# Performance work log

Hardware: AMD Instinct MI355X
Metric: run time of the kernel (lower is better)

The kernel has to match this reference:

```python
import jax, jax.numpy as jnp
import numpy as np

N = 50000
E = 800000
D_IN = 256
D_OUT = 256
ALPHA = 0.5


def setup_inputs() -> dict:
    key = jax.random.key(0)
    k1, k2, k3, k4, k5, k6 = jax.random.split(key, 6)
    stdv = 1.0 / np.sqrt(D_OUT)
    return {
        "input": jax.random.normal(k1, (N, D_IN), dtype=jnp.float32),
        "adj_src": jax.random.randint(k2, (E,), 0, N, dtype=jnp.int64),
        "adj_dst": jax.random.randint(k3, (E,), 0, N, dtype=jnp.int64),
        "adj_w": jax.random.uniform(k4, (E,), dtype=jnp.float32),
        "init_input": jax.random.normal(k5, (N, D_OUT), dtype=jnp.float32),
        "weight": jax.random.uniform(k6, (D_IN, D_OUT), dtype=jnp.float32,
                                     minval=-stdv, maxval=stdv),
    }


def reference(input, adj_src, adj_dst, adj_w, init_input, weight):
    # support = input @ W          [N, D_OUT] (dense GEMM)
    support = jnp.matmul(input, weight)
    # spmm: out[dst] += w * support[src]   (COO aggregate)
    msgs = support[adj_src] * adj_w[:, None]          # [E, D_OUT]
    agg = jax.ops.segment_sum(msgs, adj_dst, num_segments=N)  # [N, D_OUT]
    # alpha-blended residual + ReLU (bias=False, act=ReLU)
    out = agg * ALPHA + init_input * (1.0 - ALPHA)
    return jax.nn.relu(out)
```

## Files before the change

kernel.cpp:

```cpp
#include <hip/hip_runtime.h>
#include <hip/hip_fp16.h>

#define ALPHA 0.5f

typedef short short8v __attribute__((ext_vector_type(8)));
typedef float f32x4 __attribute__((ext_vector_type(4)));

__device__ __forceinline__ unsigned short f2bf(float f) {
  union { float f; unsigned u; } v; v.f = f;
  unsigned r = v.u + 0x7FFFu + ((v.u >> 16) & 1u);
  return (unsigned short)(r >> 16);
}
__device__ __forceinline__ float bf2f(unsigned short u) {
  union { unsigned u; float f; } v; v.u = ((unsigned)u) << 16;
  return v.f;
}
__device__ __forceinline__ float unpack_w(unsigned p) {
  return __half2float(__ushort_as_half((unsigned short)((p & 0x7FFFu) << 1)));
}

__global__ __launch_bounds__(256) void prep_small(
    const float* __restrict__ W, unsigned short* __restrict__ Wt,
    int* __restrict__ deg, int N) {
  const int tid = threadIdx.x;
  const int bid = blockIdx.x;
  if (bid < 256) {
    __shared__ float tile[16][17];
    const int kb = (bid & 15) * 16, nb = (bid >> 4) * 16;
    const int tx = tid & 15, ty = tid >> 4;
    tile[ty][tx] = W[(kb + ty) * 256 + nb + tx];
    __syncthreads();
    Wt[(nb + ty) * 256 + kb + tx] = f2bf(tile[tx][ty]);
  } else {
    const int i4 = (bid - 256) * 256 + tid;
    const int base = i4 * 4;
    if (base + 3 < N) *reinterpret_cast<int4*>(&deg[base]) = make_int4(0, 0, 0, 0);
    else for (int j = 0; j < 4; ++j) if (base + j < N) deg[base + j] = 0;
  }
}

__global__ __launch_bounds__(256) void gemm_hist(
    const float* __restrict__ A, const unsigned short* __restrict__ Wt,
    unsigned short* __restrict__ C, int M,
    const int* __restrict__ dst, int* __restrict__ deg, int E, int GB, int HB) {
  __shared__ char smem[2][24576];
  const int tid = threadIdx.x;
  const int bid = blockIdx.x;

  if (bid >= GB) {
    const int hgid = (bid - GB) * 256 + tid;
    const int hstride = HB * 256;
    const int E4 = E & ~3;
    for (int i = hgid * 4; i < E4; i += hstride * 4) {
      int4 d = *reinterpret_cast<const int4*>(&dst[i]);
      atomicAdd(&deg[d.x], 1); atomicAdd(&deg[d.y], 1);
      atomicAdd(&deg[d.z], 1); atomicAdd(&deg[d.w], 1);
    }
    if (hgid < (E - E4)) atomicAdd(&deg[dst[E4 + hgid]], 1);
    return;
  }

  const int lane = tid & 63;
  const int w = tid >> 6;
  const int wm = w >> 1, wn = w & 1;
  const int row0 = bid * 128;

  f32x4 acc[4][8];
  #pragma unroll
  for (int m = 0; m < 4; ++m)
    #pragma unroll
    for (int n = 0; n < 8; ++n) acc[m][n] = (f32x4){0.f, 0.f, 0.f, 0.f};

  const int aR = tid >> 1;
  const int aKs = (tid & 1) * 16;
  const int aRow = (row0 + aR < M) ? (row0 + aR) : (M - 1);
  const float* aP = A + (size_t)aRow * 256 + aKs;
  const int aWrOff = (aR >> 4) * 1024 + (aKs >> 3) * 256 + (aR & 15) * 16;

  int cur = 0;
  {
    float4 av[4];
    #pragma unroll
    for (int j = 0; j < 4; ++j) av[j] = *reinterpret_cast<const float4*>(aP + j * 4);
    #pragma unroll
    for (int i = 0; i < 4; ++i) {
      int s = w * 4 + i;
      const unsigned short* g = Wt + (size_t)(s * 16 + (lane & 15)) * 256 + (lane >> 4) * 8;
      __builtin_amdgcn_global_load_lds(
          (const __attribute__((address_space(1))) void*)g,
          (__attribute__((address_space(3))) void*)(&smem[0][8192 + s * 1024]),
          16, 0, 0);
    }
    unsigned short ab[16];
    #pragma unroll
    for (int j = 0; j < 4; ++j) {
      ab[j * 4 + 0] = f2bf(av[j].x); ab[j * 4 + 1] = f2bf(av[j].y);
      ab[j * 4 + 2] = f2bf(av[j].z); ab[j * 4 + 3] = f2bf(av[j].w);
    }
    *reinterpret_cast<short8v*>(&smem[0][aWrOff])       = *reinterpret_cast<short8v*>(&ab[0]);
    *reinterpret_cast<short8v*>(&smem[0][aWrOff + 256]) = *reinterpret_cast<short8v*>(&ab[8]);
    __syncthreads();
  }

  #pragma unroll
  for (int t = 0; t < 8; ++t) {
    float4 av[4];
    const bool pf = (t < 7);
    if (pf) {
      const int k0 = (t + 1) * 32;
      #pragma unroll
      for (int j = 0; j < 4; ++j) av[j] = *reinterpret_cast<const float4*>(aP + k0 + j * 4);
      #pragma unroll
      for (int i = 0; i < 4; ++i) {
        int s = w * 4 + i;
        const unsigned short* g = Wt + (size_t)(s * 16 + (lane & 15)) * 256 + k0 + (lane >> 4) * 8;
        __builtin_amdgcn_global_load_lds(
            (const __attribute__((address_space(1))) void*)g,
            (__attribute__((address_space(3))) void*)(&smem[cur ^ 1][8192 + s * 1024]),
            16, 0, 0);
      }
    }
    short8v af[4], bfv[8];
    #pragma unroll
    for (int m = 0; m < 4; ++m)
      af[m] = *reinterpret_cast<const short8v*>(&smem[cur][(wm * 4 + m) * 1024 + lane * 16]);
    #pragma unroll
    for (int n = 0; n < 8; ++n)
      bfv[n] = *reinterpret_cast<const short8v*>(&smem[cur][8192 + (wn * 8 + n) * 1024 + lane * 16]);
    #pragma unroll
    for (int m = 0; m < 4; ++m)
      #pragma unroll
      for (int n = 0; n < 8; ++n)
        acc[m][n] = __builtin_amdgcn_mfma_f32_16x16x32_bf16(af[m], bfv[n], acc[m][n], 0, 0, 0);
    if (pf) {
      unsigned short ab[16];
      #pragma unroll
      for (int j = 0; j < 4; ++j) {
        ab[j * 4 + 0] = f2bf(av[j].x); ab[j * 4 + 1] = f2bf(av[j].y);
        ab[j * 4 + 2] = f2bf(av[j].z); ab[j * 4 + 3] = f2bf(av[j].w);
      }
      *reinterpret_cast<short8v*>(&smem[cur ^ 1][aWrOff])       = *reinterpret_cast<short8v*>(&ab[0]);
      *reinterpret_cast<short8v*>(&smem[cur ^ 1][aWrOff + 256]) = *reinterpret_cast<short8v*>(&ab[8]);
    }
    __syncthreads();
    cur ^= 1;
  }

  #pragma unroll
  for (int m = 0; m < 4; ++m) {
    #pragma unroll
    for (int n = 0; n < 8; ++n) {
      const int col = wn * 128 + n * 16 + (lane & 15);
      #pragma unroll
      for (int r = 0; r < 4; ++r) {
        const int row = row0 + wm * 64 + m * 16 + (lane >> 4) * 4 + r;
        if (row < M) C[(size_t)row * 256 + col] = f2bf(acc[m][n][r]);
      }
    }
  }
}

__global__ __launch_bounds__(256) void scan_pass1(const int* __restrict__ deg,
                                                  int* __restrict__ excl,
                                                  int* __restrict__ partial, int N) {
  const int tid = threadIdx.x;
  const int base = blockIdx.x * 1024 + tid * 4;
  int4 v = make_int4(0, 0, 0, 0);
  if (base + 3 < N) v = *reinterpret_cast<const int4*>(&deg[base]);
  else {
    if (base + 0 < N) v.x = deg[base + 0];
    if (base + 1 < N) v.y = deg[base + 1];
    if (base + 2 < N) v.z = deg[base + 2];
  }
  const int s = v.x + v.y + v.z + v.w;
  const int lane = tid & 63, wid = tid >> 6;
  int ps = s;
  #pragma unroll
  for (int off = 1; off < 64; off <<= 1) {
    int t = __shfl_up(ps, off, 64);
    if (lane >= off) ps += t;
  }
  __shared__ int wsum[4];
  if (lane == 63) wsum[wid] = ps;
  __syncthreads();
  int woff = 0;
  #pragma unroll
  for (int w2 = 0; w2 < 4; ++w2) woff += (w2 < wid) ? wsum[w2] : 0;
  const int texcl = woff + ps - s;
  int4 e = make_int4(texcl, texcl + v.x, texcl + v.x + v.y, texcl + v.x + v.y + v.z);
  if (base + 3 < N) *reinterpret_cast<int4*>(&excl[base]) = e;
  else {
    if (base + 0 < N) excl[base + 0] = e.x;
    if (base + 1 < N) excl[base + 1] = e.y;
    if (base + 2 < N) excl[base + 2] = e.z;
  }
  if (tid == 255) partial[blockIdx.x] = woff + ps;
}

__global__ __launch_bounds__(256) void scan_pass2(const int* __restrict__ excl,
                                                  const int* __restrict__ partial,
                                                  int* __restrict__ row_ptr,
                                                  int* __restrict__ cursor,
                                                  int N, int NB, int E) {
  __shared__ int s_off;
  const int tid = threadIdx.x;
  if (tid < 64) {
    int v = (tid < NB && tid < (int)blockIdx.x) ? partial[tid] : 0;
    #pragma unroll
    for (int off = 1; off < 64; off <<= 1) v += __shfl_xor(v, off, 64);
    if (tid == 0) s_off = v;
  }
  if (blockIdx.x == 0 && tid == 0) row_ptr[N] = E;
  __syncthreads();
  const int off = s_off;
  const int base = blockIdx.x * 1024 + tid * 4;
  if (base + 3 < N) {
    int4 v = *reinterpret_cast<const int4*>(&excl[base]);
    v.x += off; v.y += off; v.z += off; v.w += off;
    *reinterpret_cast<int4*>(&row_ptr[base]) = v;
    *reinterpret_cast<int4*>(&cursor[base]) = v;
  } else {
    for (int j = 0; j < 4; ++j)
      if (base + j < N) { int v = excl[base + j] + off; row_ptr[base + j] = v; cursor[base + j] = v; }
  }
}

__global__ __launch_bounds__(256) void reindex_edges(
    const int* __restrict__ src, const int* __restrict__ dst,
    const float* __restrict__ w, int* __restrict__ cursor,
    unsigned* __restrict__ edges, int E) {
  int i = (blockIdx.x * blockDim.x + threadIdx.x) * 4;
  if (i + 3 < E) {
    int4 sv = *reinterpret_cast<const int4*>(&src[i]);
    int4 dv = *reinterpret_cast<const int4*>(&dst[i]);
    float4 wv = *reinterpret_cast<const float4*>(&w[i]);
    int s_[4] = {sv.x, sv.y, sv.z, sv.w};
    int d_[4] = {dv.x, dv.y, dv.z, dv.w};
    float w_[4] = {wv.x, wv.y, wv.z, wv.w};
    #pragma unroll
    for (int j = 0; j < 4; ++j) {
      int slot = atomicAdd(&cursor[d_[j]], 1);
      unsigned hb = __half_as_ushort(__float2half(w_[j] * ALPHA));
      edges[slot] = ((unsigned)s_[j] << 15) | (hb >> 1);
    }
  } else {
    for (; i < E; ++i) {
      int slot = atomicAdd(&cursor[dst[i]], 1);
      unsigned hb = __half_as_ushort(__float2half(w[i] * ALPHA));
      edges[slot] = ((unsigned)src[i] << 15) | (hb >> 1);
    }
  }
}

__global__ __launch_bounds__(256) void aggregate(
    const unsigned short* __restrict__ support,
    const int* __restrict__ row_ptr,
    const unsigned* __restrict__ edges,
    const float* __restrict__ init, float* __restrict__ out, int N) {
  int node = blockIdx.x * 4 + (threadIdx.x >> 6);
  if (node >= N) return;
  int lane = threadIdx.x & 63;
  int start = row_ptr[node];
  int cnt = row_ptr[node + 1] - start;

  float4 ini = *reinterpret_cast<const float4*>(&init[(size_t)node * 256 + lane * 4]);

  float4 acc = make_float4(0.f, 0.f, 0.f, 0.f);
  int e = 0;
  for (; e + 7 < cnt; e += 8) {
    unsigned p[8];
    #pragma unroll
    for (int j = 0; j < 8; ++j) p[j] = edges[start + e + j];
    ushort4 v[8];
    #pragma unroll
    for (int j = 0; j < 8; ++j)
      v[j] = *reinterpret_cast<const ushort4*>(&support[(size_t)(p[j] >> 15) * 256 + lane * 4]);
    #pragma unroll
    for (int j = 0; j < 8; ++j) {
      float wj = unpack_w(p[j]);
      acc.x += wj * bf2f(v[j].x);
      acc.y += wj * bf2f(v[j].y);
      acc.z += wj * bf2f(v[j].z);
      acc.w += wj * bf2f(v[j].w);
    }
  }
  for (; e < cnt; ++e) {
    unsigned p = edges[start + e];
    ushort4 v = *reinterpret_cast<const ushort4*>(&support[(size_t)(p >> 15) * 256 + lane * 4]);
    float wj = unpack_w(p);
    acc.x += wj * bf2f(v.x); acc.y += wj * bf2f(v.y);
    acc.z += wj * bf2f(v.z); acc.w += wj * bf2f(v.w);
  }
  float4 o;
  o.x = fmaxf(acc.x + (1.f - ALPHA) * ini.x, 0.f);
  o.y = fmaxf(acc.y + (1.f - ALPHA) * ini.y, 0.f);
  o.z = fmaxf(acc.z + (1.f - ALPHA) * ini.z, 0.f);
  o.w = fmaxf(acc.w + (1.f - ALPHA) * ini.w, 0.f);
  *reinterpret_cast<float4*>(&out[(size_t)node * 256 + lane * 4]) = o;
}

extern "C" void kernel_launch(void* const* d_in, const int* in_sizes, int n_in,
                              void* d_out, int out_size, void* d_ws, size_t ws_size,
                              hipStream_t stream) {
  const float* input   = (const float*)d_in[0];
  const int*   adj_src = (const int*)d_in[1];
  const int*   adj_dst = (const int*)d_in[2];
  const float* adj_w   = (const float*)d_in[3];
  const float* init_in = (const float*)d_in[4];
  const float* weight  = (const float*)d_in[5];
  float* out = (float*)d_out;

  const int N = in_sizes[0] / 256;
  const int E = in_sizes[1];

  char* ws = (char*)d_ws;
  unsigned short* support = (unsigned short*)ws; ws += (size_t)N * 256 * 2;
  unsigned short* Wt      = (unsigned short*)ws; ws += 256 * 256 * 2;
  int* deg     = (int*)ws; ws += (size_t)N * 4;
  int* row_ptr = (int*)ws; ws += (size_t)(N + 1) * 4;
  int* cursor  = (int*)ws; ws += (size_t)N * 4;
  int* excl    = (int*)ws; ws += (size_t)N * 4;
  int* partial = (int*)ws; ws += 256;
  unsigned* edges = (unsigned*)ws; ws += (size_t)E * 4;

  const int NB = (N + 1023) / 1024;
  const int GB = (N + 127) / 128;
  const int HB = 800;

  prep_small<<<256 + (N / 4 + 255) / 256, 256, 0, stream>>>(weight, Wt, deg, N);

  gemm_hist<<<GB + HB, 256, 0, stream>>>(input, Wt, support, N,
                                         adj_dst, deg, E, GB, HB);

  scan_pass1<<<NB, 256, 0, stream>>>(deg, excl, partial, N);
  scan_pass2<<<NB, 256, 0, stream>>>(excl, partial, row_ptr, cursor, N, NB, E);
  reindex_edges<<<(E / 4 + 255) / 256, 256, 0, stream>>>(adj_src, adj_dst, adj_w, cursor, edges, E);

  aggregate<<<(N + 3) / 4, 256, 0, stream>>>(support, row_ptr, edges, init_in, out, N);
}
```

Measured before the change: 173.2 us.

## Merge scan passes into lookback scan and precompute bf16 residual alongside GEMM

Replaces the two-kernel prefix scan over node degrees with a single-pass decoupled lookback scan using global flags, removing one launch and the intermediate buffer. Adds extra blocks to the GEMM/histogram launch that convert init_input to pre-scaled bf16, so the aggregate kernel reads half the residual bytes. The conversion adds extra global traffic that must overlap with the GEMM to pay off, and the residual loses precision by being stored in bf16. The histogram block count is reduced to make room.

```diff
diff --git a/kernel.cpp b/kernel.cpp
--- a/kernel.cpp
+++ b/kernel.cpp
@@ -21,7 +21,7 @@
 
 __global__ __launch_bounds__(256) void prep_small(
     const float* __restrict__ W, unsigned short* __restrict__ Wt,
-    int* __restrict__ deg, int N) {
+    int* __restrict__ deg, int* __restrict__ scanmeta, int N) {
   const int tid = threadIdx.x;
   const int bid = blockIdx.x;
   if (bid < 256) {
@@ -32,8 +32,8 @@
     __syncthreads();
     Wt[(nb + ty) * 256 + kb + tx] = f2bf(tile[tx][ty]);
   } else {
-    const int i4 = (bid - 256) * 256 + tid;
-    const int base = i4 * 4;
+    if (bid == 256 && tid < 128) scanmeta[tid] = 0;
+    const int base = ((bid - 256) * 256 + tid) * 4;
     if (base + 3 < N) *reinterpret_cast<int4*>(&deg[base]) = make_int4(0, 0, 0, 0);
     else for (int j = 0; j < 4; ++j) if (base + j < N) deg[base + j] = 0;
   }
@@ -42,11 +42,28 @@
 __global__ __launch_bounds__(256) void gemm_hist(
     const float* __restrict__ A, const unsigned short* __restrict__ Wt,
     unsigned short* __restrict__ C, int M,
-    const int* __restrict__ dst, int* __restrict__ deg, int E, int GB, int HB) {
+    const int* __restrict__ dst, int* __restrict__ deg, int E,
+    const float* __restrict__ init, unsigned short* __restrict__ init_bf, int n8i,
+    int GB, int HB, int CB) {
   __shared__ char smem[2][24576];
   const int tid = threadIdx.x;
   const int bid = blockIdx.x;
 
+  if (bid >= GB + HB) {
+    const int cgid = (bid - GB - HB) * 256 + tid;
+    const int cstride = CB * 256;
+    for (int i = cgid; i < n8i; i += cstride) {
+      float4 a = *reinterpret_cast<const float4*>(&init[i * 8]);
+      float4 b = *reinterpret_cast<const float4*>(&init[i * 8 + 4]);
+      unsigned short o[8] = {
+        f2bf(a.x * (1.f - ALPHA)), f2bf(a.y * (1.f - ALPHA)),
+        f2bf(a.z * (1.f - ALPHA)), f2bf(a.w * (1.f - ALPHA)),
+        f2bf(b.x * (1.f - ALPHA)), f2bf(b.y * (1.f - ALPHA)),
+        f2bf(b.z * (1.f - ALPHA)), f2bf(b.w * (1.f - ALPHA))};
+      *reinterpret_cast<short8v*>(&init_bf[i * 8]) = *reinterpret_cast<short8v*>(o);
+    }
+    return;
+  }
   if (bid >= GB) {
     const int hgid = (bid - GB) * 256 + tid;
     const int hstride = HB * 256;
@@ -160,11 +177,16 @@
   }
 }
 
-__global__ __launch_bounds__(256) void scan_pass1(const int* __restrict__ deg,
-                                                  int* __restrict__ excl,
-                                                  int* __restrict__ partial, int N) {
+__global__ __launch_bounds__(256) void scan_lookback(
+    const int* __restrict__ deg, int* __restrict__ row_ptr, int* __restrict__ cursor,
+    int* __restrict__ scanmeta ,
+    int N, int E, int NB) {
+  int* flags = scanmeta;
+  int* aggv  = scanmeta + 64;
   const int tid = threadIdx.x;
-  const int base = blockIdx.x * 1024 + tid * 4;
+  const int bid = blockIdx.x;
+  const int base = bid * 1024 + tid * 4;
+
   int4 v = make_int4(0, 0, 0, 0);
   if (base + 3 < N) v = *reinterpret_cast<const int4*>(&deg[base]);
   else {
@@ -181,47 +203,44 @@
     if (lane >= off) ps += t;
   }
   __shared__ int wsum[4];
+  __shared__ int s_off;
   if (lane == 63) wsum[wid] = ps;
   __syncthreads();
   int woff = 0;
   #pragma unroll
   for (int w2 = 0; w2 < 4; ++w2) woff += (w2 < wid) ? wsum[w2] : 0;
   const int texcl = woff + ps - s;
-  int4 e = make_int4(texcl, texcl + v.x, texcl + v.x + v.y, texcl + v.x + v.y + v.z);
-  if (base + 3 < N) *reinterpret_cast<int4*>(&excl[base]) = e;
-  else {
-    if (base + 0 < N) excl[base + 0] = e.x;
-    if (base + 1 < N) excl[base + 1] = e.y;
-    if (base + 2 < N) excl[base + 2] = e.z;
-  }
-  if (tid == 255) partial[blockIdx.x] = woff + ps;
-}
-
-__global__ __launch_bounds__(256) void scan_pass2(const int* __restrict__ excl,
-                                                  const int* __restrict__ partial,
-                                                  int* __restrict__ row_ptr,
-                                                  int* __restrict__ cursor,
-                                                  int N, int NB, int E) {
-  __shared__ int s_off;
-  const int tid = threadIdx.x;
+
+  if (tid == 0) {
+    int total = wsum[0] + wsum[1] + wsum[2] + wsum[3];
+    atomicExch(&aggv[bid], total);
+    __threadfence();
+    atomicExch(&flags[bid], 1);
+  }
+  if (bid == 0 && tid == 0) row_ptr[N] = E;
+
   if (tid < 64) {
-    int v = (tid < NB && tid < (int)blockIdx.x) ? partial[tid] : 0;
-    #pragma unroll
-    for (int off = 1; off < 64; off <<= 1) v += __shfl_xor(v, off, 64);
-    if (tid == 0) s_off = v;
-  }
-  if (blockIdx.x == 0 && tid == 0) row_ptr[N] = E;
+    int a = 0;
+    if (tid < bid) {
+      while (atomicAdd(&flags[tid], 0) == 0) { }
+      a = atomicAdd(&aggv[tid], 0);
+    }
+    #pragma unroll
+    for (int m = 1; m < 64; m <<= 1) a += __shfl_xor(a, m, 64);
+    if (tid == 0) s_off = a;
+  }
   __syncthreads();
   const int off = s_off;
-  const int base = blockIdx.x * 1024 + tid * 4;
+
+  int4 e = make_int4(texcl + off, texcl + off + v.x,
+                     texcl + off + v.x + v.y, texcl + off + v.x + v.y + v.z);
   if (base + 3 < N) {
-    int4 v = *reinterpret_cast<const int4*>(&excl[base]);
-    v.x += off; v.y += off; v.z += off; v.w += off;
-    *reinterpret_cast<int4*>(&row_ptr[base]) = v;
-    *reinterpret_cast<int4*>(&cursor[base]) = v;
+    *reinterpret_cast<int4*>(&row_ptr[base]) = e;
+    *reinterpret_cast<int4*>(&cursor[base]) = e;
   } else {
+    int ev[4] = {e.x, e.y, e.z, e.w};
     for (int j = 0; j < 4; ++j)
-      if (base + j < N) { int v = excl[base + j] + off; row_ptr[base + j] = v; cursor[base + j] = v; }
+      if (base + j < N) { row_ptr[base + j] = ev[j]; cursor[base + j] = ev[j]; }
   }
 }
 
@@ -256,14 +275,14 @@
     const unsigned short* __restrict__ support,
     const int* __restrict__ row_ptr,
     const unsigned* __restrict__ edges,
-    const float* __restrict__ init, float* __restrict__ out, int N) {
+    const unsigned short* __restrict__ init_bf, float* __restrict__ out, int N) {
   int node = blockIdx.x * 4 + (threadIdx.x >> 6);
   if (node >= N) return;
   int lane = threadIdx.x & 63;
   int start = row_ptr[node];
   int cnt = row_ptr[node + 1] - start;
 
-  float4 ini = *reinterpret_cast<const float4*>(&init[(size_t)node * 256 + lane * 4]);
+  ushort4 ib = *reinterpret_cast<const ushort4*>(&init_bf[(size_t)node * 256 + lane * 4]);
 
   float4 acc = make_float4(0.f, 0.f, 0.f, 0.f);
   int e = 0;
@@ -292,10 +311,10 @@
     acc.z += wj * bf2f(v.z); acc.w += wj * bf2f(v.w);
   }
   float4 o;
-  o.x = fmaxf(acc.x + (1.f - ALPHA) * ini.x, 0.f);
-  o.y = fmaxf(acc.y + (1.f - ALPHA) * ini.y, 0.f);
-  o.z = fmaxf(acc.z + (1.f - ALPHA) * ini.z, 0.f);
-  o.w = fmaxf(acc.w + (1.f - ALPHA) * ini.w, 0.f);
+  o.x = fmaxf(acc.x + bf2f(ib.x), 0.f);
+  o.y = fmaxf(acc.y + bf2f(ib.y), 0.f);
+  o.z = fmaxf(acc.z + bf2f(ib.z), 0.f);
+  o.w = fmaxf(acc.w + bf2f(ib.w), 0.f);
   *reinterpret_cast<float4*>(&out[(size_t)node * 256 + lane * 4]) = o;
 }
 
@@ -315,26 +334,29 @@
 
   char* ws = (char*)d_ws;
   unsigned short* support = (unsigned short*)ws; ws += (size_t)N * 256 * 2;
+  unsigned short* init_bf = (unsigned short*)ws; ws += (size_t)N * 256 * 2;
   unsigned short* Wt      = (unsigned short*)ws; ws += 256 * 256 * 2;
-  int* deg     = (int*)ws; ws += (size_t)N * 4;
-  int* row_ptr = (int*)ws; ws += (size_t)(N + 1) * 4;
-  int* cursor  = (int*)ws; ws += (size_t)N * 4;
-  int* excl    = (int*)ws; ws += (size_t)N * 4;
-  int* partial = (int*)ws; ws += 256;
+  int* deg      = (int*)ws; ws += (size_t)N * 4;
+  int* row_ptr  = (int*)ws; ws += (size_t)(N + 1) * 4;
+  int* cursor   = (int*)ws; ws += (size_t)N * 4;
+  int* scanmeta = (int*)ws; ws += 128 * 4;
   unsigned* edges = (unsigned*)ws; ws += (size_t)E * 4;
 
   const int NB = (N + 1023) / 1024;
   const int GB = (N + 127) / 128;
-  const int HB = 800;
-
-  prep_small<<<256 + (N / 4 + 255) / 256, 256, 0, stream>>>(weight, Wt, deg, N);
-
-  gemm_hist<<<GB + HB, 256, 0, stream>>>(input, Wt, support, N,
-                                         adj_dst, deg, E, GB, HB);
-
-  scan_pass1<<<NB, 256, 0, stream>>>(deg, excl, partial, N);
-  scan_pass2<<<NB, 256, 0, stream>>>(excl, partial, row_ptr, cursor, N, NB, E);
+  const int HB = 640;
+  const int CB = 320;
+  const int n8i = N * 256 / 8;
+
+  prep_small<<<256 + (N / 4 + 255) / 256, 256, 0, stream>>>(weight, Wt, deg, scanmeta, N);
+
+  gemm_hist<<<GB + HB + CB, 256, 0, stream>>>(input, Wt, support, N,
+                                              adj_dst, deg, E,
+                                              init_in, init_bf, n8i, GB, HB, CB);
+
+  scan_lookback<<<NB, 256, 0, stream>>>(deg, row_ptr, cursor, scanmeta, N, E, NB);
+
   reindex_edges<<<(E / 4 + 255) / 256, 256, 0, stream>>>(adj_src, adj_dst, adj_w, cursor, edges, E);
 
-  aggregate<<<(N + 3) / 4, 256, 0, stream>>>(support, row_ptr, edges, init_in, out, N);
-}
+  aggregate<<<(N + 3) / 4, 256, 0, stream>>>(support, row_ptr, edges, init_bf, out, N);
+}
```

Measured after the change: 193.7 us. +11.8%, slower.
